# Optimization experiments

Hardware: AMD Instinct MI355X
Metric: run time of the kernel (lower is better)

## Reference

```python
import jax, jax.numpy as jnp
import numpy as np

LORA_RANK = 16
LORA_ALPHA = 32
CHUNK_SIZE = 256
TTT_LR = 0.01
CLIP_THRESHOLD = 1.0
SCALING = LORA_ALPHA / LORA_RANK
LN_EPS = 1e-5


def setup_inputs() -> dict:
    key = jax.random.key(0)
    ks = jax.random.split(key, 5)
    B, S, K, H = 2, 8192, 1024, 1024
    x = jax.random.normal(ks[0], (B, S, K), dtype=jnp.float32)
    Wb = jax.random.normal(ks[1], (H, K), dtype=jnp.float32) / np.sqrt(K)
    init_A = jax.random.normal(ks[2], (H, LORA_RANK), dtype=jnp.float32) * 0.01
    init_B = jax.random.normal(ks[3], (LORA_RANK, K), dtype=jnp.float32) * 0.01
    ln_gamma = jnp.ones((K,), dtype=jnp.float32)
    ln_beta = jnp.zeros((K,), dtype=jnp.float32)
    Wp = jax.random.normal(ks[4], (H, K), dtype=jnp.float32) / np.sqrt(K)
    return {"x": x, "Wb": Wb, "init_A": init_A, "init_B": init_B,
            "ln_gamma": ln_gamma, "ln_beta": ln_beta, "Wp": Wp}


def _forward(x, Wb, init_A, init_B, ln_gamma, ln_beta, Wp):
    B_sz, Seq, k_dim = x.shape
    h_dim = Wb.shape[0]
    r = init_A.shape[1]
    nc = Seq // CHUNK_SIZE  # Seq chosen divisible; pad_len == 0

    base_out = x @ Wb.T  # [B, S, H]

    # --- target construction under no_grad: LayerNorm + left-shift ---
    xd = jax.lax.stop_gradient(x)
    mu = jnp.mean(xd, axis=-1, keepdims=True)
    var = jnp.mean((xd - mu) ** 2, axis=-1, keepdims=True)
    xn = (xd - mu) * jax.lax.rsqrt(var + LN_EPS) * ln_gamma + ln_beta
    shifted = jnp.pad(xn[:, 1:, :], ((0, 0), (0, 1), (0, 0)))
    shifted = jax.lax.stop_gradient(shifted)

    V = shifted @ Wp.T  # [B, S, H]

    Z = x.reshape(B_sz * nc, CHUNK_SIZE, k_dim)
    Vc = V.reshape(B_sz * nc, CHUNK_SIZE, h_dim)

    # per-chunk fast-weight deltas
    proj_in = Z @ init_B.T                                # [BC, C, r]
    dA = jnp.einsum('bch,bcr->bhr', Vc, proj_in)          # [BC, H, r]
    proj_err = Vc @ init_A                                # [BC, C, r]
    dB = jnp.einsum('bcr,bck->brk', proj_err, Z)          # [BC, r, K]

    dA = dA.reshape(B_sz, nc, h_dim, r)
    dB = dB.reshape(B_sz, nc, r, k_dim)

    # exclusive cross-chunk cumsum
    accA = jnp.cumsum(dA, axis=1)
    accB = jnp.cumsum(dB, axis=1)
    accA = jnp.concatenate([jnp.zeros_like(accA[:, :1]), accA[:, :-1]], axis=1)
    accB = jnp.concatenate([jnp.zeros_like(accB[:, :1]), accB[:, :-1]], axis=1)

    lr = TTT_LR * SCALING
    rawA = (lr * accA).reshape(-1, h_dim, r)
    rawB = (lr * accB).reshape(-1, r, k_dim)

    # joint norm clip (norm_type=2)
    norm_sq = (jnp.sum(rawA.astype(jnp.float32) ** 2, axis=(-2, -1), keepdims=True)
               + jnp.sum(rawB.astype(jnp.float32) ** 2, axis=(-2, -1), keepdims=True))
    total_norm = jnp.sqrt(norm_sq)
    coef = jnp.minimum(CLIP_THRESHOLD / (total_norm + 1e-6), 1.0).astype(rawA.dtype)

    A_eff = init_A[None] - rawA * coef  # [BC, H, r]
    B_eff = init_B[None] - rawB * coef  # [BC, r, K]

    mid = jnp.einsum('bck,brk->bcr', Z, B_eff)          # [BC, C, r]
    lora = jnp.einsum('bcr,bhr->bch', mid, A_eff)       # [BC, C, H]
    lora = lora.reshape(B_sz, Seq, h_dim)

    return base_out + lora * SCALING


def reference(x, Wb, init_A, init_B, ln_gamma, ln_beta, Wp):
    return _forward(x, Wb, init_A, init_B, ln_gamma, ln_beta, Wp)
```

## Files before the change

### kernel.cpp

```cpp
#include <hip/hip_runtime.h>

typedef __attribute__((ext_vector_type(8))) short s16x8;
typedef __attribute__((ext_vector_type(4))) float f32x4;
typedef __attribute__((ext_vector_type(2))) float f32x2;
typedef unsigned short u16;

#define B_SZ 2
#define SEQ 8192
#define KD 1024
#define HD 1024
#define RK 16
#define CH 256
#define NCH 64
static constexpr float LR_SC = 0.02f;
static constexpr float SCALE_OUT = 2.0f;

__device__ __forceinline__ u16 f2b(float f) {
  union { float f; unsigned int u; } c; c.f = f;
  unsigned int u = c.u;
  unsigned int r = (u + 0x7fffu + ((u >> 16) & 1u)) >> 16;
  return (u16)r;
}
__device__ __forceinline__ float b2f(u16 v) {
  union { unsigned int u; float f; } c; c.u = ((unsigned int)v) << 16; return c.f;
}
__device__ __forceinline__ void async16(const u16* g, u16* l) {
  __builtin_amdgcn_global_load_lds((const __attribute__((address_space(1))) void*)g,
                                   (__attribute__((address_space(3))) void*)l, 16, 0, 0);
}

__global__ __launch_bounds__(256) void cvt_all(const float* __restrict__ Wb,
                                               const float* __restrict__ Wp,
                                               const float* __restrict__ initB,
                                               u16* __restrict__ Wbb,
                                               u16* __restrict__ Wpb,
                                               u16* __restrict__ iBb) {
  int bid = blockIdx.x;
  const float* src; u16* dst; int base;
  if (bid < 1024)      { src = Wb;    dst = Wbb; base = bid; }
  else if (bid < 2048) { src = Wp;    dst = Wpb; base = bid - 1024; }
  else                 { src = initB; dst = iBb; base = bid - 2048; }
  int i = (base * 256 + threadIdx.x) * 4;
  float4 v = *(const float4*)(src + i);
  ushort4 o; o.x = f2b(v.x); o.y = f2b(v.y); o.z = f2b(v.z); o.w = f2b(v.w);
  *(ushort4*)(dst + i) = o;
}

__global__ __launch_bounds__(256) void wpat_part(const float* __restrict__ initA,
                                                 const float* __restrict__ Wp,
                                                 float* __restrict__ part) {
  int t = threadIdx.x;
  int k = blockIdx.x * 256 + t;
  int hseg = blockIdx.y;
  __shared__ float Asm[64 * 16];
  *(float4*)&Asm[t * 4] = *(const float4*)&initA[(size_t)hseg * 1024 + t * 4];
  __syncthreads();
  float acc[16];
  #pragma unroll
  for (int j = 0; j < 16; j++) acc[j] = 0.f;
  const float* wp = Wp + (size_t)hseg * 64 * KD + k;
  #pragma unroll 8
  for (int hh = 0; hh < 64; hh++) {
    float w = wp[(size_t)hh * KD];
    const float4* ar = (const float4*)&Asm[hh * 16];
    #pragma unroll
    for (int qq = 0; qq < 4; qq++) {
      float4 a = ar[qq];
      acc[qq*4+0] += w * a.x; acc[qq*4+1] += w * a.y;
      acc[qq*4+2] += w * a.z; acc[qq*4+3] += w * a.w;
    }
  }
  float* o = part + ((size_t)hseg * 1024 + k) * 16;
  #pragma unroll
  for (int qq = 0; qq < 4; qq++) {
    float4 r; r.x = acc[qq*4]; r.y = acc[qq*4+1]; r.z = acc[qq*4+2]; r.w = acc[qq*4+3];
    *(float4*)&o[qq * 4] = r;
  }
}

__global__ __launch_bounds__(256) void wpat_reduce(const float* __restrict__ part,
                                                   u16* __restrict__ WpAT) {
  int idx = blockIdx.x * 256 + threadIdx.x;
  int k = idx & 1023, r = idx >> 10;
  float s = 0.f;
  #pragma unroll
  for (int seg = 0; seg < 16; seg++)
    s += part[((size_t)seg * 1024 + k) * 16 + r];
  WpAT[(size_t)r * KD + k] = f2b(s);
}

__global__ __launch_bounds__(256) void ln_shift(const float* __restrict__ x,
                                                const float* __restrict__ gamma,
                                                const float* __restrict__ beta,
                                                u16* __restrict__ xb,
                                                u16* __restrict__ shb) {
  int row = blockIdx.x;
  int t = threadIdx.x;
  int s = row & (SEQ - 1);
  const float* xr = x + (size_t)row * KD;
  float4 v = *(const float4*)(xr + t * 4);
  ushort4 o; o.x = f2b(v.x); o.y = f2b(v.y); o.z = f2b(v.z); o.w = f2b(v.w);
  *(ushort4*)(xb + (size_t)row * KD + t * 4) = o;

  if (s == 0) {
    ushort4 z; z.x = 0; z.y = 0; z.z = 0; z.w = 0;
    *(ushort4*)(shb + ((size_t)row + SEQ - 1) * KD + t * 4) = z;
    return;
  }
  float s1 = v.x + v.y + v.z + v.w;
  float s2 = v.x * v.x + v.y * v.y + v.z * v.z + v.w * v.w;
  #pragma unroll
  for (int off = 32; off > 0; off >>= 1) {
    s1 += __shfl_down(s1, off);
    s2 += __shfl_down(s2, off);
  }
  __shared__ float red[8];
  int wave = t >> 6, lane = t & 63;
  if (lane == 0) { red[wave * 2] = s1; red[wave * 2 + 1] = s2; }
  __syncthreads();
  float sum = red[0] + red[2] + red[4] + red[6];
  float ssq = red[1] + red[3] + red[5] + red[7];
  float mu = sum * (1.0f / KD);
  float var = ssq * (1.0f / KD) - mu * mu;
  float rstd = rsqrtf(var + 1e-5f);
  float4 g = *(const float4*)(gamma + t * 4);
  float4 bb = *(const float4*)(beta + t * 4);
  ushort4 so;
  so.x = f2b((v.x - mu) * rstd * g.x + bb.x);
  so.y = f2b((v.y - mu) * rstd * g.y + bb.y);
  so.z = f2b((v.z - mu) * rstd * g.z + bb.z);
  so.w = f2b((v.w - mu) * rstd * g.w + bb.w);
  *(ushort4*)(shb + (size_t)(row - 1) * KD + t * 4) = so;
}

__global__ __launch_bounds__(256, 2) void gemm_fused(const u16* __restrict__ A,
                                                     const u16* __restrict__ Bm,
                                                     const u16* __restrict__ mid2,
                                                     const u16* __restrict__ Aef,
                                                     float* __restrict__ C) {
  constexpr int BM = 128, BN = 128, BK = 64, N = HD, Kd = KD;
  __shared__ u16 As[BM * BK];
  __shared__ u16 Bs[BN * BK];
  int tid = threadIdx.x;
  int lane = tid & 63, wave = tid >> 6;
  int lb = blockIdx.x + 8 * blockIdx.y;
  int q = lb & 7, t = lb >> 3;
  int mb = q * 16 + (t >> 3);
  int nb = t & 7;
  int m0 = mb * 128, n0 = nb * 128;
  int wm = (wave >> 1) * 64, wn = (wave & 1) * 64;
  int lr = lane & 15;
  int qd = lane >> 4;
  int sw = lr & 7;
  int slot0 = ((qd ^ sw) * 8);
  int slot1 = (((4 + qd) ^ sw) * 8);
  f32x4 acc[4][4] = {};

  const u16* gbase; u16* lbase;
  if (wave < 2) { gbase = A + (size_t)(m0 + wave * 64) * Kd; lbase = As + wave * 64 * BK; }
  else          { gbase = Bm + (size_t)(n0 + (wave - 2) * 64) * Kd; lbase = Bs + (wave - 2) * 64 * BK; }
  int srow = lane >> 3;
  int scol = ((lane & 7) ^ srow) * 8;
  const u16* gsrc = gbase + (size_t)srow * Kd + scol;

  for (int k0 = 0; k0 < Kd; k0 += BK) {
    #pragma unroll
    for (int i = 0; i < 8; i++)
      async16(gsrc + (size_t)i * 8 * Kd, lbase + i * 512);
    gsrc += BK;
    __syncthreads();
    s16x8 af[4], bfr[4];
    #pragma unroll
    for (int i = 0; i < 4; i++) af[i] = *(const s16x8*)(As + (wm + i * 16 + lr) * BK + slot0);
    #pragma unroll
    for (int j = 0; j < 4; j++) bfr[j] = *(const s16x8*)(Bs + (wn + j * 16 + lr) * BK + slot0);
    #pragma unroll
    for (int i = 0; i < 4; i++)
      #pragma unroll
      for (int j = 0; j < 4; j++)
        acc[i][j] = __builtin_amdgcn_mfma_f32_16x16x32_bf16(af[i], bfr[j], acc[i][j], 0, 0, 0);
    #pragma unroll
    for (int i = 0; i < 4; i++) af[i] = *(const s16x8*)(As + (wm + i * 16 + lr) * BK + slot1);
    #pragma unroll
    for (int j = 0; j < 4; j++) bfr[j] = *(const s16x8*)(Bs + (wn + j * 16 + lr) * BK + slot1);
    #pragma unroll
    for (int i = 0; i < 4; i++)
      #pragma unroll
      for (int j = 0; j < 4; j++)
        acc[i][j] = __builtin_amdgcn_mfma_f32_16x16x32_bf16(af[i], bfr[j], acc[i][j], 0, 0, 0);
    __syncthreads();
  }

  {
    int chunk = m0 >> 8;
    const u16* abase = Aef + (size_t)chunk * (HD * RK);
    int klane = lane >> 4;
    s16x8 am2[4], bn2[4];
    #pragma unroll
    for (int i = 0; i < 4; i++) {
      if (klane < 2)
        am2[i] = *(const s16x8*)(mid2 + (size_t)(m0 + wm + i * 16 + lr) * RK + klane * 8);
      else { s16x8 z = {}; am2[i] = z; }
    }
    #pragma unroll
    for (int j = 0; j < 4; j++) {
      if (klane < 2)
        bn2[j] = *(const s16x8*)(abase + (size_t)(n0 + wn + j * 16 + lr) * RK + klane * 8);
      else { s16x8 z = {}; bn2[j] = z; }
    }
    #pragma unroll
    for (int i = 0; i < 4; i++)
      #pragma unroll
      for (int j = 0; j < 4; j++)
        acc[i][j] = __builtin_amdgcn_mfma_f32_16x16x32_bf16(am2[i], bn2[j], acc[i][j], 0, 0, 0);
  }

  int rb = (lane >> 4) * 4, cc = lane & 15;
  #pragma unroll
  for (int i = 0; i < 4; i++)
    #pragma unroll
    for (int j = 0; j < 4; j++)
      #pragma unroll
      for (int p = 0; p < 4; p++)
        C[(size_t)(m0 + wm + i * 16 + rb + p) * N + (n0 + wn + j * 16 + cc)] = acc[i][j][p];
}

__global__ __launch_bounds__(256) void rank16_proj(const u16* __restrict__ xb,
                                                   const u16* __restrict__ shb,
                                                   const u16* __restrict__ iBb,
                                                   const u16* __restrict__ WpAT,
                                                   float* __restrict__ pin,
                                                   float* __restrict__ per) {
  const u16* X; const u16* W; float* O;
  if (blockIdx.z == 0) { X = xb; W = iBb; O = pin; }
  else                 { X = shb; W = WpAT; O = per; }
  int wave = threadIdx.x >> 6, lane = threadIdx.x & 63;
  int m0 = (blockIdx.x * 4 + wave) * 16;
  int lr = lane & 15, lk = (lane >> 4) * 8;
  const u16* xp = X + (size_t)(m0 + lr) * KD + lk;
  const u16* wp = W + (size_t)lr * KD + lk;
  f32x4 acc = {};
  #pragma unroll 8
  for (int k0 = 0; k0 < KD; k0 += 32) {
    s16x8 a = *(const s16x8*)xp;
    s16x8 b = *(const s16x8*)wp;
    acc = __builtin_amdgcn_mfma_f32_16x16x32_bf16(a, b, acc, 0, 0, 0);
    xp += 32; wp += 32;
  }
  int rb = (lane >> 4) * 4, cc = lane & 15;
  #pragma unroll
  for (int p = 0; p < 4; p++)
    O[(size_t)(m0 + rb + p) * RK + cc] = acc[p];
}

__global__ __launch_bounds__(256) void rank16_mid(const u16* __restrict__ xb,
                                                  const u16* __restrict__ Bef,
                                                  u16* __restrict__ mid2) {
  int wave = threadIdx.x >> 6, lane = threadIdx.x & 63;
  int m0 = (blockIdx.x * 4 + wave) * 16;
  int chunk = m0 >> 8;
  int lr = lane & 15, lk = (lane >> 4) * 8;
  const u16* xp = xb + (size_t)(m0 + lr) * KD + lk;
  const u16* wp = Bef + (size_t)chunk * (RK * KD) + (size_t)lr * KD + lk;
  f32x4 acc = {};
  #pragma unroll 8
  for (int k0 = 0; k0 < KD; k0 += 32) {
    s16x8 a = *(const s16x8*)xp;
    s16x8 b = *(const s16x8*)wp;
    acc = __builtin_amdgcn_mfma_f32_16x16x32_bf16(a, b, acc, 0, 0, 0);
    xp += 32; wp += 32;
  }
  int rb = (lane >> 4) * 4, cc = lane & 15;
  #pragma unroll
  for (int p = 0; p < 4; p++)
    mid2[(size_t)(m0 + rb + p) * RK + cc] = f2b(SCALE_OUT * acc[p]);
}

__global__ __launch_bounds__(256) void gk_kernel(const u16* __restrict__ xb,
                                                 const u16* __restrict__ shb,
                                                 const float* __restrict__ pin,
                                                 const float* __restrict__ per,
                                                 float* __restrict__ G,
                                                 float* __restrict__ dB) {
  int tile = blockIdx.x;
  int chunk = blockIdx.y;
  int which = blockIdx.z;
  int t = threadIdx.x;
  __shared__ float P[CH * RK];
  const float* psrc = which ? per : pin;
  for (int i = t; i < 1024; i += 256)
    *(float4*)&P[i * 4] = *(const float4*)&psrc[(size_t)chunk * 4096 + i * 4];
  __syncthreads();
  f32x2 acc[8];
  #pragma unroll
  for (int j = 0; j < 8; j++) acc[j] = (f32x2){0.f, 0.f};
  int col = tile * 256 + t;
  const u16* src = (which ? xb : shb) + (size_t)chunk * CH * KD + col;
  #pragma unroll 4
  for (int c = 0; c < 256; c++) {
    float v = b2f(src[(size_t)c * 1024]);
    f32x2 vv = {v, v};
    const f32x2* pr = (const f32x2*)&P[c * 16];
    #pragma unroll
    for (int qq = 0; qq < 8; qq++)
      acc[qq] += vv * pr[qq];
  }
  float* o = (which ? dB : G) + (size_t)chunk * 16384 + col;
  #pragma unroll
  for (int j = 0; j < 8; j++) {
    o[(size_t)(2 * j) * 1024] = acc[j][0];
    o[(size_t)(2 * j + 1) * 1024] = acc[j][1];
  }
}

__global__ __launch_bounds__(256) void cumsum_kernel(const float* __restrict__ G,
                                                     const float* __restrict__ dB,
                                                     u16* __restrict__ rawG,
                                                     float* __restrict__ rawB) {
  int idx = blockIdx.x * 256 + threadIdx.x;
  int which = idx >> 15;
  int rem = idx & 32767;
  int b = rem >> 14;
  int e = rem & 16383;
  size_t base = (size_t)b * 32 * 16384 + e;
  if (which == 0) {
    float run = 0.f;
    for (int i = 0; i < 32; i++) {
      size_t off = base + (size_t)i * 16384;
      float nv = G[off];
      rawG[off] = f2b(LR_SC * run);
      run += nv;
    }
  } else {
    float run = 0.f;
    for (int i = 0; i < 32; i++) {
      size_t off = base + (size_t)i * 16384;
      float nv = dB[off];
      rawB[off] = LR_SC * run;
      run += nv;
    }
  }
}

__global__ __launch_bounds__(256) void dagemm(const u16* __restrict__ Wpb,
                                              const u16* __restrict__ rawG,
                                              float* __restrict__ rawA) {
  int wave = threadIdx.x >> 6, lane = threadIdx.x & 63;
  int m0 = (blockIdx.x * 4 + wave) * 16;
  int chunk = blockIdx.y;
  int lr = lane & 15, lk = (lane >> 4) * 8;
  const u16* ap = Wpb + (size_t)(m0 + lr) * KD + lk;
  const u16* bp = rawG + (size_t)chunk * 16384 + (size_t)lr * KD + lk;
  f32x4 acc = {};
  #pragma unroll 8
  for (int k0 = 0; k0 < KD; k0 += 32) {
    s16x8 a = *(const s16x8*)ap;
    s16x8 b = *(const s16x8*)bp;
    acc = __builtin_amdgcn_mfma_f32_16x16x32_bf16(a, b, acc, 0, 0, 0);
    ap += 32; bp += 32;
  }
  int rb = (lane >> 4) * 4, cc = lane & 15;
  #pragma unroll
  for (int p = 0; p < 4; p++)
    rawA[(size_t)chunk * 16384 + (size_t)(m0 + rb + p) * RK + cc] = acc[p];
}

__global__ __launch_bounds__(1024) void coef_eff(const float* __restrict__ initA,
                                                 const float* __restrict__ initB,
                                                 const float* __restrict__ rawA,
                                                 const float* __restrict__ rawB,
                                                 u16* __restrict__ Aef,
                                                 u16* __restrict__ Bef) {
  int chunk = blockIdx.x, t = threadIdx.x;
  const float* a = rawA + (size_t)chunk * 16384;
  const float* b = rawB + (size_t)chunk * 16384;
  float s = 0.f;
  #pragma unroll
  for (int i = t * 4; i < 16384; i += 4096) {
    float4 v = *(const float4*)(a + i);
    s += v.x*v.x + v.y*v.y + v.z*v.z + v.w*v.w;
    float4 w = *(const float4*)(b + i);
    s += w.x*w.x + w.y*w.y + w.z*w.z + w.w*w.w;
  }
  #pragma unroll
  for (int off = 32; off > 0; off >>= 1) s += __shfl_down(s, off);
  __shared__ float red[16];
  int wave = t >> 6, lane = t & 63;
  if (lane == 0) red[wave] = s;
  __syncthreads();
  float tot = 0.f;
  #pragma unroll
  for (int w = 0; w < 16; w++) tot += red[w];
  float cf = fminf(1.0f / (sqrtf(tot) + 1e-6f), 1.0f);
  u16* ao = Aef + (size_t)chunk * 16384;
  u16* bo = Bef + (size_t)chunk * 16384;
  #pragma unroll
  for (int i = t * 4; i < 16384; i += 4096) {
    float4 iv = *(const float4*)(initA + i);
    float4 rv = *(const float4*)(a + i);
    ushort4 r;
    r.x = f2b(iv.x - rv.x * cf); r.y = f2b(iv.y - rv.y * cf);
    r.z = f2b(iv.z - rv.z * cf); r.w = f2b(iv.w - rv.w * cf);
    *(ushort4*)(ao + i) = r;
    float4 iw = *(const float4*)(initB + i);
    float4 rw = *(const float4*)(b + i);
    ushort4 rr;
    rr.x = f2b(iw.x - rw.x * cf); rr.y = f2b(iw.y - rw.y * cf);
    rr.z = f2b(iw.z - rw.z * cf); rr.w = f2b(iw.w - rw.w * cf);
    *(ushort4*)(bo + i) = rr;
  }
}

extern "C" void kernel_launch(void* const* d_in, const int* in_sizes, int n_in,
                              void* d_out, int out_size, void* d_ws, size_t ws_size,
                              hipStream_t stream) {
  (void)in_sizes; (void)n_in; (void)out_size; (void)ws_size;
  const float* x     = (const float*)d_in[0];
  const float* Wb    = (const float*)d_in[1];
  const float* initA = (const float*)d_in[2];
  const float* initB = (const float*)d_in[3];
  const float* gamma = (const float*)d_in[4];
  const float* beta  = (const float*)d_in[5];
  const float* Wp    = (const float*)d_in[6];
  float* out = (float*)d_out;

  char* ws = (char*)d_ws;
  size_t off = 0;
  auto alloc = [&](size_t bytes) -> void* {
    void* p = ws + off;
    off = (off + bytes + 255) & ~(size_t)255;
    return p;
  };
  const size_t ROWS = (size_t)B_SZ * SEQ;
  u16* xb    = (u16*)alloc(ROWS * KD * 2);
  u16* shb   = (u16*)alloc(ROWS * KD * 2);
  u16* Wbb   = (u16*)alloc((size_t)HD * KD * 2);
  u16* Wpb   = (u16*)alloc((size_t)HD * KD * 2);
  u16* iBb   = (u16*)alloc((size_t)RK * KD * 2);
  u16* WpAT  = (u16*)alloc((size_t)RK * KD * 2);
  float* wpart = (float*)alloc((size_t)16 * KD * RK * 4);
  float* pin = (float*)alloc((size_t)NCH * CH * RK * 4);
  float* per = (float*)alloc((size_t)NCH * CH * RK * 4);
  float* G   = (float*)alloc((size_t)NCH * 16384 * 4);
  float* dB  = (float*)alloc((size_t)NCH * 16384 * 4);
  u16* rawG  = (u16*)alloc((size_t)NCH * 16384 * 2);
  float* rawB= (float*)alloc((size_t)NCH * 16384 * 4);
  float* rawA= (float*)alloc((size_t)NCH * 16384 * 4);
  u16* Aef   = (u16*)alloc((size_t)NCH * 16384 * 2);
  u16* Bef   = (u16*)alloc((size_t)NCH * 16384 * 2);
  u16* mid2  = (u16*)alloc(ROWS * RK * 2);

  cvt_all<<<2064, 256, 0, stream>>>(Wb, Wp, initB, Wbb, Wpb, iBb);
  wpat_part<<<dim3(4, 16), 256, 0, stream>>>(initA, Wp, wpart);
  wpat_reduce<<<64, 256, 0, stream>>>(wpart, WpAT);
  ln_shift<<<ROWS, 256, 0, stream>>>(x, gamma, beta, xb, shb);
  rank16_proj<<<dim3(256, 1, 2), 256, 0, stream>>>(xb, shb, iBb, WpAT, pin, per);
  gk_kernel<<<dim3(4, NCH, 2), 256, 0, stream>>>(xb, shb, pin, per, G, dB);
  cumsum_kernel<<<256, 256, 0, stream>>>(G, dB, rawG, rawB);
  dagemm<<<dim3(16, NCH), 256, 0, stream>>>(Wpb, rawG, rawA);
  coef_eff<<<NCH, 1024, 0, stream>>>(initA, initB, rawA, rawB, Aef, Bef);
  rank16_mid<<<256, 256, 0, stream>>>(xb, Bef, mid2);
  gemm_fused<<<dim3(8, 128), 256, 0, stream>>>(xb, Wbb, mid2, Aef, out);
}
```

Baseline: 281.5 us.

## Merge independent small kernels into phased launches to cut launch gaps

Restructures the pre-GEMM pipeline into five phase kernels that each run two independent pieces of work via block-index dispatch. The Wp·A reduction, weight conversion and LayerNorm/shift share one launch, the projections are interleaved with the gk and cumsum stages, and the cumsum is split between G and dB. This reduces the launch count from eleven to eight and lets independent work overlap inside a launch. In exchange, shared-memory use is sized for the largest branch and the blocks within a launch are heterogeneous.

New measurement: 289.5 us. 2.9% more time.

```diff
diff --git a/kernel.cpp b/kernel.cpp
--- a/kernel.cpp
+++ b/kernel.cpp
@@ -29,13 +29,14 @@
                                    (__attribute__((address_space(3))) void*)l, 16, 0, 0);
 }
 
-__global__ __launch_bounds__(256) void cvt_all(const float* __restrict__ Wb,
-                                               const float* __restrict__ Wp,
-                                               const float* __restrict__ initB,
-                                               u16* __restrict__ Wbb,
-                                               u16* __restrict__ Wpb,
-                                               u16* __restrict__ iBb) {
-  int bid = blockIdx.x;
+
+__device__ __forceinline__ void body_cvt(int bid,
+                                         const float* __restrict__ Wb,
+                                         const float* __restrict__ Wp,
+                                         const float* __restrict__ initB,
+                                         u16* __restrict__ Wbb,
+                                         u16* __restrict__ Wpb,
+                                         u16* __restrict__ iBb) {
   const float* src; u16* dst; int base;
   if (bid < 1024)      { src = Wb;    dst = Wbb; base = bid; }
   else if (bid < 2048) { src = Wp;    dst = Wpb; base = bid - 1024; }
@@ -46,56 +47,99 @@
   *(ushort4*)(dst + i) = o;
 }
 
-__global__ __launch_bounds__(256) void wpat_part(const float* __restrict__ initA,
-                                                 const float* __restrict__ Wp,
-                                                 float* __restrict__ part) {
+__device__ __forceinline__ void body_proj(const u16* __restrict__ X,
+                                          const u16* __restrict__ W,
+                                          float* __restrict__ O, int bid) {
+  int wave = threadIdx.x >> 6, lane = threadIdx.x & 63;
+  int m0 = (bid * 4 + wave) * 16;
+  int lr = lane & 15, lk = (lane >> 4) * 8;
+  const u16* xp = X + (size_t)(m0 + lr) * KD + lk;
+  const u16* wp = W + (size_t)lr * KD + lk;
+  f32x4 acc = {};
+  #pragma unroll 8
+  for (int k0 = 0; k0 < KD; k0 += 32) {
+    s16x8 a = *(const s16x8*)xp;
+    s16x8 b = *(const s16x8*)wp;
+    acc = __builtin_amdgcn_mfma_f32_16x16x32_bf16(a, b, acc, 0, 0, 0);
+    xp += 32; wp += 32;
+  }
+  int rb = (lane >> 4) * 4, cc = lane & 15;
+  #pragma unroll
+  for (int p = 0; p < 4; p++)
+    O[(size_t)(m0 + rb + p) * RK + cc] = acc[p];
+}
+
+__device__ __forceinline__ void body_gk(int tile, int chunk,
+                                        const u16* __restrict__ src0,
+                                        const float* __restrict__ psrc,
+                                        float* __restrict__ dst) {
   int t = threadIdx.x;
-  int k = blockIdx.x * 256 + t;
-  int hseg = blockIdx.y;
-  __shared__ float Asm[64 * 16];
-  *(float4*)&Asm[t * 4] = *(const float4*)&initA[(size_t)hseg * 1024 + t * 4];
+  __shared__ float P[CH * RK];
+  for (int i = t; i < 1024; i += 256)
+    *(float4*)&P[i * 4] = *(const float4*)&psrc[(size_t)chunk * 4096 + i * 4];
   __syncthreads();
-  float acc[16];
-  #pragma unroll
-  for (int j = 0; j < 16; j++) acc[j] = 0.f;
-  const float* wp = Wp + (size_t)hseg * 64 * KD + k;
-  #pragma unroll 8
-  for (int hh = 0; hh < 64; hh++) {
-    float w = wp[(size_t)hh * KD];
-    const float4* ar = (const float4*)&Asm[hh * 16];
+  f32x2 acc[8];
+  #pragma unroll
+  for (int j = 0; j < 8; j++) acc[j] = (f32x2){0.f, 0.f};
+  int col = tile * 256 + t;
+  const u16* src = src0 + (size_t)chunk * CH * KD + col;
+  #pragma unroll 4
+  for (int c = 0; c < 256; c++) {
+    float v = b2f(src[(size_t)c * 1024]);
+    f32x2 vv = {v, v};
+    const f32x2* pr = (const f32x2*)&P[c * 16];
+    #pragma unroll
+    for (int qq = 0; qq < 8; qq++)
+      acc[qq] += vv * pr[qq];
+  }
+  float* o = dst + (size_t)chunk * 16384 + col;
+  #pragma unroll
+  for (int j = 0; j < 8; j++) {
+    o[(size_t)(2 * j) * 1024] = acc[j][0];
+    o[(size_t)(2 * j + 1) * 1024] = acc[j][1];
+  }
+}
+
+__global__ __launch_bounds__(256) void phase1(
+    const float* __restrict__ x, const float* __restrict__ gamma, const float* __restrict__ beta,
+    const float* __restrict__ Wb, const float* __restrict__ Wp, const float* __restrict__ initB,
+    const float* __restrict__ initA,
+    u16* __restrict__ xb, u16* __restrict__ shb,
+    u16* __restrict__ Wbb, u16* __restrict__ Wpb, u16* __restrict__ iBb,
+    float* __restrict__ part) {
+  int bid = blockIdx.x;
+  int t = threadIdx.x;
+  if (bid < 64) {
+    int k = (bid & 3) * 256 + t;
+    int hseg = bid >> 2;
+    __shared__ float Asm[64 * 16];
+    *(float4*)&Asm[t * 4] = *(const float4*)&initA[(size_t)hseg * 1024 + t * 4];
+    __syncthreads();
+    float acc[16];
+    #pragma unroll
+    for (int j = 0; j < 16; j++) acc[j] = 0.f;
+    const float* wp = Wp + (size_t)hseg * 64 * KD + k;
+    #pragma unroll 8
+    for (int hh = 0; hh < 64; hh++) {
+      float w = wp[(size_t)hh * KD];
+      const float4* ar = (const float4*)&Asm[hh * 16];
+      #pragma unroll
+      for (int qq = 0; qq < 4; qq++) {
+        float4 a = ar[qq];
+        acc[qq*4+0] += w * a.x; acc[qq*4+1] += w * a.y;
+        acc[qq*4+2] += w * a.z; acc[qq*4+3] += w * a.w;
+      }
+    }
+    float* o = part + ((size_t)hseg * 1024 + k) * 16;
     #pragma unroll
     for (int qq = 0; qq < 4; qq++) {
-      float4 a = ar[qq];
-      acc[qq*4+0] += w * a.x; acc[qq*4+1] += w * a.y;
-      acc[qq*4+2] += w * a.z; acc[qq*4+3] += w * a.w;
+      float4 r; r.x = acc[qq*4]; r.y = acc[qq*4+1]; r.z = acc[qq*4+2]; r.w = acc[qq*4+3];
+      *(float4*)&o[qq * 4] = r;
     }
-  }
-  float* o = part + ((size_t)hseg * 1024 + k) * 16;
-  #pragma unroll
-  for (int qq = 0; qq < 4; qq++) {
-    float4 r; r.x = acc[qq*4]; r.y = acc[qq*4+1]; r.z = acc[qq*4+2]; r.w = acc[qq*4+3];
-    *(float4*)&o[qq * 4] = r;
-  }
-}
-
-__global__ __launch_bounds__(256) void wpat_reduce(const float* __restrict__ part,
-                                                   u16* __restrict__ WpAT) {
-  int idx = blockIdx.x * 256 + threadIdx.x;
-  int k = idx & 1023, r = idx >> 10;
-  float s = 0.f;
-  #pragma unroll
-  for (int seg = 0; seg < 16; seg++)
-    s += part[((size_t)seg * 1024 + k) * 16 + r];
-  WpAT[(size_t)r * KD + k] = f2b(s);
-}
-
-__global__ __launch_bounds__(256) void ln_shift(const float* __restrict__ x,
-                                                const float* __restrict__ gamma,
-                                                const float* __restrict__ beta,
-                                                u16* __restrict__ xb,
-                                                u16* __restrict__ shb) {
-  int row = blockIdx.x;
-  int t = threadIdx.x;
+    return;
+  }
+  if (bid < 2128) { body_cvt(bid - 64, Wb, Wp, initB, Wbb, Wpb, iBb); return; }
+  int row = bid - 2128;
   int s = row & (SEQ - 1);
   const float* xr = x + (size_t)row * KD;
   float4 v = *(const float4*)(xr + t * 4);
@@ -131,6 +175,163 @@
   so.z = f2b((v.z - mu) * rstd * g.z + bb.z);
   so.w = f2b((v.w - mu) * rstd * g.w + bb.w);
   *(ushort4*)(shb + (size_t)(row - 1) * KD + t * 4) = so;
+}
+
+__global__ __launch_bounds__(256) void phase2(const u16* __restrict__ xb,
+                                              const u16* __restrict__ iBb,
+                                              float* __restrict__ pin,
+                                              const float* __restrict__ part,
+                                              u16* __restrict__ WpAT) {
+  int bid = blockIdx.x;
+  if (bid < 256) { body_proj(xb, iBb, pin, bid); return; }
+  int idx = (bid - 256) * 256 + threadIdx.x;
+  int k = idx & 1023, r = idx >> 10;
+  float s = 0.f;
+  #pragma unroll
+  for (int seg = 0; seg < 16; seg++)
+    s += part[((size_t)seg * 1024 + k) * 16 + r];
+  WpAT[(size_t)r * KD + k] = f2b(s);
+}
+
+__global__ __launch_bounds__(256) void phase3(const u16* __restrict__ shb,
+                                              const float* __restrict__ pin,
+                                              float* __restrict__ G,
+                                              const u16* __restrict__ WpAT,
+                                              float* __restrict__ per) {
+  int bid = blockIdx.x;
+  if (bid < 256) { body_gk(bid & 3, bid >> 2, shb, pin, G); return; }
+  body_proj(shb, WpAT, per, bid - 256);
+}
+
+__global__ __launch_bounds__(256) void phase4(const u16* __restrict__ xb,
+                                              const float* __restrict__ per,
+                                              float* __restrict__ dB,
+                                              const float* __restrict__ G,
+                                              u16* __restrict__ rawG) {
+  int bid = blockIdx.x;
+  if (bid < 256) { body_gk(bid & 3, bid >> 2, xb, per, dB); return; }
+  int idx = (bid - 256) * 256 + threadIdx.x;
+  int b = idx >> 14;
+  int e = idx & 16383;
+  size_t base = (size_t)b * 32 * 16384 + e;
+  float run = 0.f;
+  #pragma unroll 8
+  for (int i = 0; i < 32; i++) {
+    size_t off = base + (size_t)i * 16384;
+    float nv = G[off];
+    rawG[off] = f2b(LR_SC * run);
+    run += nv;
+  }
+}
+
+__global__ __launch_bounds__(256) void phase5(const u16* __restrict__ Wpb,
+                                              const u16* __restrict__ rawG,
+                                              float* __restrict__ rawA,
+                                              const float* __restrict__ dB,
+                                              float* __restrict__ rawB) {
+  int bid = blockIdx.x;
+  if (bid < 1024) {
+    int wave = threadIdx.x >> 6, lane = threadIdx.x & 63;
+    int m0 = ((bid & 15) * 4 + wave) * 16;
+    int chunk = bid >> 4;
+    int lr = lane & 15, lk = (lane >> 4) * 8;
+    const u16* ap = Wpb + (size_t)(m0 + lr) * KD + lk;
+    const u16* bp = rawG + (size_t)chunk * 16384 + (size_t)lr * KD + lk;
+    f32x4 acc = {};
+    #pragma unroll 8
+    for (int k0 = 0; k0 < KD; k0 += 32) {
+      s16x8 a = *(const s16x8*)ap;
+      s16x8 b = *(const s16x8*)bp;
+      acc = __builtin_amdgcn_mfma_f32_16x16x32_bf16(a, b, acc, 0, 0, 0);
+      ap += 32; bp += 32;
+    }
+    int rb = (lane >> 4) * 4, cc = lane & 15;
+    #pragma unroll
+    for (int p = 0; p < 4; p++)
+      rawA[(size_t)chunk * 16384 + (size_t)(m0 + rb + p) * RK + cc] = acc[p];
+    return;
+  }
+  int idx = (bid - 1024) * 256 + threadIdx.x;
+  int b = idx >> 14;
+  int e = idx & 16383;
+  size_t base = (size_t)b * 32 * 16384 + e;
+  float run = 0.f;
+  #pragma unroll 8
+  for (int i = 0; i < 32; i++) {
+    size_t off = base + (size_t)i * 16384;
+    float nv = dB[off];
+    rawB[off] = LR_SC * run;
+    run += nv;
+  }
+}
+
+__global__ __launch_bounds__(1024) void coef_eff(const float* __restrict__ initA,
+                                                 const float* __restrict__ initB,
+                                                 const float* __restrict__ rawA,
+                                                 const float* __restrict__ rawB,
+                                                 u16* __restrict__ Aef,
+                                                 u16* __restrict__ Bef) {
+  int chunk = blockIdx.x, t = threadIdx.x;
+  const float* a = rawA + (size_t)chunk * 16384;
+  const float* b = rawB + (size_t)chunk * 16384;
+  float s = 0.f;
+  #pragma unroll
+  for (int i = t * 4; i < 16384; i += 4096) {
+    float4 v = *(const float4*)(a + i);
+    s += v.x*v.x + v.y*v.y + v.z*v.z + v.w*v.w;
+    float4 w = *(const float4*)(b + i);
+    s += w.x*w.x + w.y*w.y + w.z*w.z + w.w*w.w;
+  }
+  #pragma unroll
+  for (int off = 32; off > 0; off >>= 1) s += __shfl_down(s, off);
+  __shared__ float red[16];
+  int wave = t >> 6, lane = t & 63;
+  if (lane == 0) red[wave] = s;
+  __syncthreads();
+  float tot = 0.f;
+  #pragma unroll
+  for (int w = 0; w < 16; w++) tot += red[w];
+  float cf = fminf(1.0f / (sqrtf(tot) + 1e-6f), 1.0f);
+  u16* ao = Aef + (size_t)chunk * 16384;
+  u16* bo = Bef + (size_t)chunk * 16384;
+  #pragma unroll
+  for (int i = t * 4; i < 16384; i += 4096) {
+    float4 iv = *(const float4*)(initA + i);
+    float4 rv = *(const float4*)(a + i);
+    ushort4 r;
+    r.x = f2b(iv.x - rv.x * cf); r.y = f2b(iv.y - rv.y * cf);
+    r.z = f2b(iv.z - rv.z * cf); r.w = f2b(iv.w - rv.w * cf);
+    *(ushort4*)(ao + i) = r;
+    float4 iw = *(const float4*)(initB + i);
+    float4 rw = *(const float4*)(b + i);
+    ushort4 rr;
+    rr.x = f2b(iw.x - rw.x * cf); rr.y = f2b(iw.y - rw.y * cf);
+    rr.z = f2b(iw.z - rw.z * cf); rr.w = f2b(iw.w - rw.w * cf);
+    *(ushort4*)(bo + i) = rr;
+  }
+}
+
+__global__ __launch_bounds__(256) void rank16_mid(const u16* __restrict__ xb,
+                                                  const u16* __restrict__ Bef,
+                                                  u16* __restrict__ mid2) {
+  int wave = threadIdx.x >> 6, lane = threadIdx.x & 63;
+  int m0 = (blockIdx.x * 4 + wave) * 16;
+  int chunk = m0 >> 8;
+  int lr = lane & 15, lk = (lane >> 4) * 8;
+  const u16* xp = xb + (size_t)(m0 + lr) * KD + lk;
+  const u16* wp = Bef + (size_t)chunk * (RK * KD) + (size_t)lr * KD + lk;
+  f32x4 acc = {};
+  #pragma unroll 8
+  for (int k0 = 0; k0 < KD; k0 += 32) {
+    s16x8 a = *(const s16x8*)xp;
+    s16x8 b = *(const s16x8*)wp;
+    acc = __builtin_amdgcn_mfma_f32_16x16x32_bf16(a, b, acc, 0, 0, 0);
+    xp += 32; wp += 32;
+  }
+  int rb = (lane >> 4) * 4, cc = lane & 15;
+  #pragma unroll
+  for (int p = 0; p < 4; p++)
+    mid2[(size_t)(m0 + rb + p) * RK + cc] = f2b(SCALE_OUT * acc[p]);
 }
 
 __global__ __launch_bounds__(256, 2) void gemm_fused(const u16* __restrict__ A,
@@ -223,192 +424,6 @@
       #pragma unroll
       for (int p = 0; p < 4; p++)
         C[(size_t)(m0 + wm + i * 16 + rb + p) * N + (n0 + wn + j * 16 + cc)] = acc[i][j][p];
-}
-
-__global__ __launch_bounds__(256) void rank16_proj(const u16* __restrict__ xb,
-                                                   const u16* __restrict__ shb,
-                                                   const u16* __restrict__ iBb,
-                                                   const u16* __restrict__ WpAT,
-                                                   float* __restrict__ pin,
-                                                   float* __restrict__ per) {
-  const u16* X; const u16* W; float* O;
-  if (blockIdx.z == 0) { X = xb; W = iBb; O = pin; }
-  else                 { X = shb; W = WpAT; O = per; }
-  int wave = threadIdx.x >> 6, lane = threadIdx.x & 63;
-  int m0 = (blockIdx.x * 4 + wave) * 16;
-  int lr = lane & 15, lk = (lane >> 4) * 8;
-  const u16* xp = X + (size_t)(m0 + lr) * KD + lk;
-  const u16* wp = W + (size_t)lr * KD + lk;
-  f32x4 acc = {};
-  #pragma unroll 8
-  for (int k0 = 0; k0 < KD; k0 += 32) {
-    s16x8 a = *(const s16x8*)xp;
-    s16x8 b = *(const s16x8*)wp;
-    acc = __builtin_amdgcn_mfma_f32_16x16x32_bf16(a, b, acc, 0, 0, 0);
-    xp += 32; wp += 32;
-  }
-  int rb = (lane >> 4) * 4, cc = lane & 15;
-  #pragma unroll
-  for (int p = 0; p < 4; p++)
-    O[(size_t)(m0 + rb + p) * RK + cc] = acc[p];
-}
-
-__global__ __launch_bounds__(256) void rank16_mid(const u16* __restrict__ xb,
-                                                  const u16* __restrict__ Bef,
-                                                  u16* __restrict__ mid2) {
-  int wave = threadIdx.x >> 6, lane = threadIdx.x & 63;
-  int m0 = (blockIdx.x * 4 + wave) * 16;
-  int chunk = m0 >> 8;
-  int lr = lane & 15, lk = (lane >> 4) * 8;
-  const u16* xp = xb + (size_t)(m0 + lr) * KD + lk;
-  const u16* wp = Bef + (size_t)chunk * (RK * KD) + (size_t)lr * KD + lk;
-  f32x4 acc = {};
-  #pragma unroll 8
-  for (int k0 = 0; k0 < KD; k0 += 32) {
-    s16x8 a = *(const s16x8*)xp;
-    s16x8 b = *(const s16x8*)wp;
-    acc = __builtin_amdgcn_mfma_f32_16x16x32_bf16(a, b, acc, 0, 0, 0);
-    xp += 32; wp += 32;
-  }
-  int rb = (lane >> 4) * 4, cc = lane & 15;
-  #pragma unroll
-  for (int p = 0; p < 4; p++)
-    mid2[(size_t)(m0 + rb + p) * RK + cc] = f2b(SCALE_OUT * acc[p]);
-}
-
-__global__ __launch_bounds__(256) void gk_kernel(const u16* __restrict__ xb,
-                                                 const u16* __restrict__ shb,
-                                                 const float* __restrict__ pin,
-                                                 const float* __restrict__ per,
-                                                 float* __restrict__ G,
-                                                 float* __restrict__ dB) {
-  int tile = blockIdx.x;
-  int chunk = blockIdx.y;
-  int which = blockIdx.z;
-  int t = threadIdx.x;
-  __shared__ float P[CH * RK];
-  const float* psrc = which ? per : pin;
-  for (int i = t; i < 1024; i += 256)
-    *(float4*)&P[i * 4] = *(const float4*)&psrc[(size_t)chunk * 4096 + i * 4];
-  __syncthreads();
-  f32x2 acc[8];
-  #pragma unroll
-  for (int j = 0; j < 8; j++) acc[j] = (f32x2){0.f, 0.f};
-  int col = tile * 256 + t;
-  const u16* src = (which ? xb : shb) + (size_t)chunk * CH * KD + col;
-  #pragma unroll 4
-  for (int c = 0; c < 256; c++) {
-    float v = b2f(src[(size_t)c * 1024]);
-    f32x2 vv = {v, v};
-    const f32x2* pr = (const f32x2*)&P[c * 16];
-    #pragma unroll
-    for (int qq = 0; qq < 8; qq++)
-      acc[qq] += vv * pr[qq];
-  }
-  float* o = (which ? dB : G) + (size_t)chunk * 16384 + col;
-  #pragma unroll
-  for (int j = 0; j < 8; j++) {
-    o[(size_t)(2 * j) * 1024] = acc[j][0];
-    o[(size_t)(2 * j + 1) * 1024] = acc[j][1];
-  }
-}
-
-__global__ __launch_bounds__(256) void cumsum_kernel(const float* __restrict__ G,
-                                                     const float* __restrict__ dB,
-                                                     u16* __restrict__ rawG,
-                                                     float* __restrict__ rawB) {
-  int idx = blockIdx.x * 256 + threadIdx.x;
-  int which = idx >> 15;
-  int rem = idx & 32767;
-  int b = rem >> 14;
-  int e = rem & 16383;
-  size_t base = (size_t)b * 32 * 16384 + e;
-  if (which == 0) {
-    float run = 0.f;
-    for (int i = 0; i < 32; i++) {
-      size_t off = base + (size_t)i * 16384;
-      float nv = G[off];
-      rawG[off] = f2b(LR_SC * run);
-      run += nv;
-    }
-  } else {
-    float run = 0.f;
-    for (int i = 0; i < 32; i++) {
-      size_t off = base + (size_t)i * 16384;
-      float nv = dB[off];
-      rawB[off] = LR_SC * run;
-      run += nv;
-    }
-  }
-}
-
-__global__ __launch_bounds__(256) void dagemm(const u16* __restrict__ Wpb,
-                                              const u16* __restrict__ rawG,
-                                              float* __restrict__ rawA) {
-  int wave = threadIdx.x >> 6, lane = threadIdx.x & 63;
-  int m0 = (blockIdx.x * 4 + wave) * 16;
-  int chunk = blockIdx.y;
-  int lr = lane & 15, lk = (lane >> 4) * 8;
-  const u16* ap = Wpb + (size_t)(m0 + lr) * KD + lk;
-  const u16* bp = rawG + (size_t)chunk * 16384 + (size_t)lr * KD + lk;
-  f32x4 acc = {};
-  #pragma unroll 8
-  for (int k0 = 0; k0 < KD; k0 += 32) {
-    s16x8 a = *(const s16x8*)ap;
-    s16x8 b = *(const s16x8*)bp;
-    acc = __builtin_amdgcn_mfma_f32_16x16x32_bf16(a, b, acc, 0, 0, 0);
-    ap += 32; bp += 32;
-  }
-  int rb = (lane >> 4) * 4, cc = lane & 15;
-  #pragma unroll
-  for (int p = 0; p < 4; p++)
-    rawA[(size_t)chunk * 16384 + (size_t)(m0 + rb + p) * RK + cc] = acc[p];
-}
-
-__global__ __launch_bounds__(1024) void coef_eff(const float* __restrict__ initA,
-                                                 const float* __restrict__ initB,
-                                                 const float* __restrict__ rawA,
-                                                 const float* __restrict__ rawB,
-                                                 u16* __restrict__ Aef,
-                                                 u16* __restrict__ Bef) {
-  int chunk = blockIdx.x, t = threadIdx.x;
-  const float* a = rawA + (size_t)chunk * 16384;
-  const float* b = rawB + (size_t)chunk * 16384;
-  float s = 0.f;
-  #pragma unroll
-  for (int i = t * 4; i < 16384; i += 4096) {
-    float4 v = *(const float4*)(a + i);
-    s += v.x*v.x + v.y*v.y + v.z*v.z + v.w*v.w;
-    float4 w = *(const float4*)(b + i);
-    s += w.x*w.x + w.y*w.y + w.z*w.z + w.w*w.w;
-  }
-  #pragma unroll
-  for (int off = 32; off > 0; off >>= 1) s += __shfl_down(s, off);
-  __shared__ float red[16];
-  int wave = t >> 6, lane = t & 63;
-  if (lane == 0) red[wave] = s;
-  __syncthreads();
-  float tot = 0.f;
-  #pragma unroll
-  for (int w = 0; w < 16; w++) tot += red[w];
-  float cf = fminf(1.0f / (sqrtf(tot) + 1e-6f), 1.0f);
-  u16* ao = Aef + (size_t)chunk * 16384;
-  u16* bo = Bef + (size_t)chunk * 16384;
-  #pragma unroll
-  for (int i = t * 4; i < 16384; i += 4096) {
-    float4 iv = *(const float4*)(initA + i);
-    float4 rv = *(const float4*)(a + i);
-    ushort4 r;
-    r.x = f2b(iv.x - rv.x * cf); r.y = f2b(iv.y - rv.y * cf);
-    r.z = f2b(iv.z - rv.z * cf); r.w = f2b(iv.w - rv.w * cf);
-    *(ushort4*)(ao + i) = r;
-    float4 iw = *(const float4*)(initB + i);
-    float4 rw = *(const float4*)(b + i);
-    ushort4 rr;
-    rr.x = f2b(iw.x - rw.x * cf); rr.y = f2b(iw.y - rw.y * cf);
-    rr.z = f2b(iw.z - rw.z * cf); rr.w = f2b(iw.w - rw.w * cf);
-    *(ushort4*)(bo + i) = rr;
-  }
 }
 
 extern "C" void kernel_launch(void* const* d_in, const int* in_sizes, int n_in,
@@ -450,14 +465,12 @@
   u16* Bef   = (u16*)alloc((size_t)NCH * 16384 * 2);
   u16* mid2  = (u16*)alloc(ROWS * RK * 2);
 
-  cvt_all<<<2064, 256, 0, stream>>>(Wb, Wp, initB, Wbb, Wpb, iBb);
-  wpat_part<<<dim3(4, 16), 256, 0, stream>>>(initA, Wp, wpart);
-  wpat_reduce<<<64, 256, 0, stream>>>(wpart, WpAT);
-  ln_shift<<<ROWS, 256, 0, stream>>>(x, gamma, beta, xb, shb);
-  rank16_proj<<<dim3(256, 1, 2), 256, 0, stream>>>(xb, shb, iBb, WpAT, pin, per);
-  gk_kernel<<<dim3(4, NCH, 2), 256, 0, stream>>>(xb, shb, pin, per, G, dB);
-  cumsum_kernel<<<256, 256, 0, stream>>>(G, dB, rawG, rawB);
-  dagemm<<<dim3(16, NCH), 256, 0, stream>>>(Wpb, rawG, rawA);
+  phase1<<<64 + 2064 + 16384, 256, 0, stream>>>(x, gamma, beta, Wb, Wp, initB, initA,
+                                                xb, shb, Wbb, Wpb, iBb, wpart);
+  phase2<<<256 + 64, 256, 0, stream>>>(xb, iBb, pin, wpart, WpAT);
+  phase3<<<256 + 256, 256, 0, stream>>>(shb, pin, G, WpAT, per);
+  phase4<<<256 + 128, 256, 0, stream>>>(xb, per, dB, G, rawG);
+  phase5<<<1024 + 128, 256, 0, stream>>>(Wpb, rawG, rawA, dB, rawB);
   coef_eff<<<NCH, 1024, 0, stream>>>(initA, initB, rawA, rawB, Aef, Bef);
   rank16_mid<<<256, 256, 0, stream>>>(xb, Bef, mid2);
   gemm_fused<<<dim3(8, 128), 256, 0, stream>>>(xb, Wbb, mid2, Aef, out);
```
